# Performance work log

Hardware: AMD Instinct MI355X
Metric: run time of the kernel (lower is better)

## Reference

```python
import jax, jax.numpy as jnp
import numpy as np

K = 7        # kernel_dim
P = 3        # padding
G = 1        # groups
EPS = 1e-5   # BatchNorm eps


def _unfold(X):
    # X: (B, C, H, W) -> patches (B, C, K*K, H, W), torch.nn.Unfold ordering (C major, then kh, kw)
    B, C, H, W = X.shape
    Xp = jnp.pad(X, ((0, 0), (0, 0), (P, P), (P, P)))
    pats = [Xp[:, :, i:i + H, j:j + W] for i in range(K) for j in range(K)]
    return jnp.stack(pats, axis=2)


def setup_inputs() -> dict:
    key = jax.random.key(0)
    ks = jax.random.split(key, 4)
    B, C, H, W = 2, 64, 128, 128
    Cr = 16  # out_dim // reduction
    return {
        "X": jax.random.normal(ks[0], (B, C, H, W), dtype=jnp.float32),
        "w_reduce": jax.random.normal(ks[1], (Cr, C), dtype=jnp.float32) * 0.05,
        "b_reduce": jnp.zeros((Cr,), dtype=jnp.float32),
        "gamma": jnp.ones((Cr,), dtype=jnp.float32),
        "beta": jnp.zeros((Cr,), dtype=jnp.float32),
        "w_span": jax.random.normal(ks[2], (K * K * G, Cr), dtype=jnp.float32) * 0.05,
        "b_span": jnp.zeros((K * K * G,), dtype=jnp.float32),
    }


def reference(X, w_reduce, b_reduce, gamma, beta, w_span, b_span):
    B, C, H, W = X.shape
    out_dim = C  # in_dim == out_dim -> initial_mapping is Identity

    # unfold (im2col): (B, G, out_dim//G, K*K, H, W)
    unfolded = _unfold(X).reshape(B, G, out_dim // G, K * K, H, W)

    # kernel generation: stride==1 -> pool is Identity
    reduced = jnp.einsum('bchw,oc->bohw', X, w_reduce) + b_reduce[None, :, None, None]
    # BatchNorm2d (training mode: batch statistics) + ReLU
    mean = reduced.mean(axis=(0, 2, 3))
    var = reduced.var(axis=(0, 2, 3))
    bn = (reduced - mean[None, :, None, None]) * jax.lax.rsqrt(var + EPS)[None, :, None, None]
    act = jax.nn.relu(bn * gamma[None, :, None, None] + beta[None, :, None, None])

    kernel = jnp.einsum('bchw,kc->bkhw', act, w_span) + b_span[None, :, None, None]
    kernel = kernel.reshape(B, G, K * K, H, W)[:, :, None]  # (B, G, 1, K*K, H, W)

    out = (kernel * unfolded).sum(axis=3)  # (B, G, out_dim//G, H, W)
    return out.reshape(B, out_dim, H, W)
```

## Files before the change

kernel.cpp:

```cpp
#include <hip/hip_runtime.h>
#include <math.h>

constexpr int B  = 2, C = 64, H = 128, W = 128;
constexpr int Cr = 16;
constexpr int K  = 7, KK = 49;
constexpr int HW  = H * W;
constexpr int CHW = C * HW;
constexpr int NPIX = B * HW;
constexpr float EPS = 1e-5f;

constexpr int R_F = NPIX * Cr;
constexpr int P_F = 512 * 32;
constexpr size_t WS_NEED = (size_t)(R_F + P_F + 64) * 4;


__global__ __launch_bounds__(256) void k_reduce_r(
    const float* __restrict__ X, const float* __restrict__ w_reduce,
    const float* __restrict__ b_reduce, float* __restrict__ r_ws,
    float* __restrict__ partial)
{
    __shared__ float wrS[Cr * C];
    __shared__ float tmpA[4][Cr][64];
    const int t = threadIdx.x;
    for (int i = t; i < Cr * C; i += 256) wrS[i] = w_reduce[i];
    __syncthreads();

    const int pixl = t & 63, cg = t >> 6;
    const int p = blockIdx.x * 64 + pixl;
    const int b = p >> 14, hw = p & (HW - 1);
    const float* xb = X + (size_t)b * CHW + hw;

    float x[16];
    #pragma unroll
    for (int i = 0; i < 16; ++i) x[i] = xb[(cg * 16 + i) * HW];

    float rp[16];
    #pragma unroll
    for (int o = 0; o < 16; ++o) rp[o] = (cg == 0) ? b_reduce[o] : 0.f;
    #pragma unroll
    for (int i = 0; i < 16; ++i) {
        const float xv = x[i];
        #pragma unroll
        for (int o = 0; o < 16; ++o)
            rp[o] = fmaf(xv, wrS[o * 64 + cg * 16 + i], rp[o]);
    }
    #pragma unroll
    for (int o = 0; o < 16; ++o) tmpA[cg][o][pixl] = rp[o];
    __syncthreads();

    float rr[4];
    #pragma unroll
    for (int j = 0; j < 4; ++j) {
        const int o = cg * 4 + j;
        rr[j] = tmpA[0][o][pixl] + tmpA[1][o][pixl] + tmpA[2][o][pixl] + tmpA[3][o][pixl];
    }
    *(float4*)&r_ws[(size_t)p * 16 + cg * 4] = make_float4(rr[0], rr[1], rr[2], rr[3]);

    float s[4], q[4];
    #pragma unroll
    for (int j = 0; j < 4; ++j) { s[j] = rr[j]; q[j] = rr[j] * rr[j]; }
    #pragma unroll
    for (int off = 32; off > 0; off >>= 1) {
        #pragma unroll
        for (int j = 0; j < 4; ++j) {
            s[j] += __shfl_down(s[j], off);
            q[j] += __shfl_down(q[j], off);
        }
    }
    if ((t & 63) == 0) {
        #pragma unroll
        for (int j = 0; j < 4; ++j) {
            partial[blockIdx.x * 32 + cg * 4 + j]      = s[j];
            partial[blockIdx.x * 32 + 16 + cg * 4 + j] = q[j];
        }
    }
}

constexpr int TLH = 8, TLW = 16;
constexpr int HR = TLH + 6, HC = TLW + 6;
constexpr int RPT = 24;
constexpr int CSP = HR * RPT + 4;
constexpr int XS3_F = 32 * CSP;
constexpr int KC3_F = KK * 128;
constexpr int SMEM3_F = XS3_F + KC3_F + 256 + 32;
constexpr int SMEM3_BYTES = SMEM3_F * 4;

__global__ __launch_bounds__(256) void k_inv3(
    const float* __restrict__ X, const float* __restrict__ r_ws,
    const float* __restrict__ partial, const float* __restrict__ gamma,
    const float* __restrict__ beta, const float* __restrict__ w_span,
    const float* __restrict__ b_span, float* __restrict__ out)
{
    extern __shared__ float smem[];
    float* Xs  = smem;
    float* kcS = Xs + XS3_F;
    float* red = kcS + KC3_F;
    float* scS = red + 256;
    float* ofS = scS + 16;

    const int t   = threadIdx.x;
    const int raw = blockIdx.x;
    const int wg  = (raw & 7) * 64 + (raw >> 3);
    const int tile = wg & 127;
    const int half = (wg >> 7) & 1;
    const int b    = wg >> 8;
    const int th0 = (tile >> 3) * TLH;
    const int tw0 = (tile & 7) * TLW;

    const int px = t & 127;
    const int h  = t >> 7;
    const int p1r = px >> 4, p1c = px & 15;
    const size_t gp = (size_t)b * HW + (size_t)(th0 + p1r) * W + (tw0 + p1c);
    const float4 r0 = *(const float4*)&r_ws[gp * 16 + 0];
    const float4 r1 = *(const float4*)&r_ws[gp * 16 + 4];
    const float4 r2 = *(const float4*)&r_ws[gp * 16 + 8];
    const float4 r3 = *(const float4*)&r_ws[gp * 16 + 12];

    {
        const int scol = t & 31;
        const int sch  = t >> 5;
        const int gw   = tw0 + scol - 3;
        const bool wok = (unsigned)gw < (unsigned)W;
        const float* xg = X + (size_t)b * CHW + (size_t)(half * 32) * HW;
        #pragma unroll
        for (int cb = 0; cb < 4; ++cb) {
            const int c = cb * 8 + sch;
            const float* xc = xg + (size_t)c * HW;
            float* xs = Xs + c * CSP + scol;
            #pragma unroll
            for (int r = 0; r < HR; ++r) {
                const int gh = th0 + r - 3;
                float v = 0.f;
                if (wok && (unsigned)gh < (unsigned)H) v = xc[gh * W + gw];
                if (scol < HC) xs[r * RPT] = v;
            }
        }
    }

    {
        const int o = t & 31, seg = t >> 5;
        float acc = 0.f;
        #pragma unroll 16
        for (int j = 0; j < 64; ++j) acc += partial[(size_t)(seg * 64 + j) * 32 + o];
        red[seg * 32 + o] = acc;
    }
    __syncthreads();
    if (t < 64) {
        const int o2 = t & 31;
        float tot = 0.f;
        #pragma unroll
        for (int g = 0; g < 8; ++g) tot += red[g * 32 + o2];
        const float sq = __shfl(tot, (t & 31) + 16);
        if (t < 16) {
            const float mean = tot / (float)NPIX;
            const float var  = sq / (float)NPIX - mean * mean;
            const float sc   = gamma[t] * rsqrtf(var + EPS);
            scS[t] = sc;
            ofS[t] = beta[t] - mean * sc;
        }
    }
    __syncthreads();

    {
        float act[16];
        const float rv[16] = {r0.x, r0.y, r0.z, r0.w, r1.x, r1.y, r1.z, r1.w,
                              r2.x, r2.y, r2.z, r2.w, r3.x, r3.y, r3.z, r3.w};
        #pragma unroll
        for (int o = 0; o < 16; ++o)
            act[o] = fmaxf(fmaf(scS[o], rv[o], ofS[o]), 0.f);
        #pragma unroll
        for (int j = 0; j < 25; ++j) {
            const int k = h * 25 + j;
            if (k < KK) {
                float v = b_span[k];
                #pragma unroll
                for (int o = 0; o < 16; ++o)
                    v = fmaf(act[o], w_span[k * 16 + o], v);
                kcS[k * 128 + px] = v;
            }
        }
    }
    __syncthreads();

    const int strip = t & 31;
    const int chg   = t >> 5;
    const int pr3 = strip >> 2, pc = (strip & 3) * 4;
    const int c0  = chg * 4;

    float acc[4][4];
    #pragma unroll
    for (int i = 0; i < 4; ++i)
        #pragma unroll
        for (int j = 0; j < 4; ++j) acc[i][j] = 0.f;

    #pragma unroll
    for (int kh = 0; kh < 7; ++kh) {
        float4 kcr[7];
        #pragma unroll
        for (int kw = 0; kw < 7; ++kw)
            kcr[kw] = *(const float4*)&kcS[(kh * 7 + kw) * 128 + pr3 * 16 + pc];
        const float* kf = (const float*)kcr;
        #pragma unroll
        for (int i = 0; i < 4; ++i) {
            const float* xr = &Xs[(c0 + i) * CSP + (pr3 + kh) * RPT + pc];
            const float4 xa = *(const float4*)&xr[0];
            const float4 xb = *(const float4*)&xr[4];
            const float4 xc = *(const float4*)&xr[8];
            const float xw[12] = {xa.x, xa.y, xa.z, xa.w,
                                  xb.x, xb.y, xb.z, xb.w,
                                  xc.x, xc.y, xc.z, xc.w};
            #pragma unroll
            for (int kw = 0; kw < 7; ++kw)
                #pragma unroll
                for (int j = 0; j < 4; ++j)
                    acc[i][j] = fmaf(kf[kw * 4 + j], xw[kw + j], acc[i][j]);
        }
    }

    float* ob = out + (size_t)b * CHW + (size_t)(half * 32 + c0) * HW
                    + (size_t)(th0 + pr3) * W + (tw0 + pc);
    #pragma unroll
    for (int i = 0; i < 4; ++i)
        *(float4*)&ob[(size_t)i * HW] = make_float4(acc[i][0], acc[i][1], acc[i][2], acc[i][3]);
}


constexpr int XS_F  = C * 196;
constexpr int KC_F  = KK * 64;
constexpr int ACT_F = Cr * 64;
constexpr int WR_F  = Cr * C;
constexpr int WSP_F = KK * Cr;
constexpr int SMEM_F = XS_F + KC_F + ACT_F + WR_F + WSP_F + KK + Cr + Cr;
constexpr int SMEM_BYTES = SMEM_F * 4;

__global__ __launch_bounds__(128) void k_reduce_stats(
    const float* __restrict__ X, const float* __restrict__ w_reduce,
    const float* __restrict__ b_reduce, float* __restrict__ partial)
{
    __shared__ float wr[WR_F];
    __shared__ float brd[Cr];
    __shared__ float tmp[2][32];
    const int t = threadIdx.x;
    for (int i = t; i < WR_F; i += 128) wr[i] = w_reduce[i];
    if (t < Cr) brd[t] = b_reduce[t];
    __syncthreads();
    const int p  = blockIdx.x * 128 + t;
    const int b  = p >> 14;
    const int hw = p & (HW - 1);
    const float* xb = X + b * CHW + hw;
    float r[Cr];
    #pragma unroll
    for (int o = 0; o < Cr; ++o) r[o] = brd[o];
    #pragma unroll 4
    for (int c = 0; c < C; ++c) {
        const float x = xb[c * HW];
        #pragma unroll
        for (int o = 0; o < Cr; ++o) r[o] = fmaf(x, wr[o * C + c], r[o]);
    }
    const int lane = t & 63, wv = t >> 6;
    #pragma unroll
    for (int o = 0; o < Cr; ++o) {
        float s = r[o], q = r[o] * r[o];
        #pragma unroll
        for (int off = 32; off > 0; off >>= 1) {
            s += __shfl_down(s, off);
            q += __shfl_down(q, off);
        }
        if (lane == 0) { tmp[wv][o] = s; tmp[wv][Cr + o] = q; }
    }
    __syncthreads();
    if (t < 32) partial[blockIdx.x * 32 + t] = tmp[0][t] + tmp[1][t];
}

__global__ __launch_bounds__(256) void k_stats_final(
    const float* __restrict__ partial, float* __restrict__ stats)
{
    __shared__ float red[256];
    __shared__ float fin[32];
    const int t = threadIdx.x;
    const int o = t & 31, g = t >> 5;
    float acc = 0.f;
    #pragma unroll 8
    for (int j = 0; j < 32; ++j) acc += partial[(g * 32 + j) * 32 + o];
    red[t] = acc;
    __syncthreads();
    if (t < 32) {
        float v = 0.f;
        #pragma unroll
        for (int g2 = 0; g2 < 8; ++g2) v += red[g2 * 32 + t];
        fin[t] = v;
    }
    __syncthreads();
    if (t < Cr) {
        const float mean = fin[t] / (float)NPIX;
        const float var  = fin[Cr + t] / (float)NPIX - mean * mean;
        stats[t]      = mean;
        stats[Cr + t] = rsqrtf(var + EPS);
    }
}

__global__ __launch_bounds__(256) void k_involution(
    const float* __restrict__ X, const float* __restrict__ w_reduce,
    const float* __restrict__ b_reduce, const float* __restrict__ gamma,
    const float* __restrict__ beta, const float* __restrict__ w_span,
    const float* __restrict__ b_span, const float* __restrict__ stats,
    float* __restrict__ out)
{
    extern __shared__ float smem[];
    float* Xs   = smem;
    float* kcS  = Xs  + XS_F;
    float* actS = kcS + KC_F;
    float* wrS  = actS + ACT_F;
    float* wspS = wrS + WR_F;
    float* bspS = wspS + WSP_F;
    float* scS  = bspS + KK;
    float* ofS  = scS + Cr;
    const int t    = threadIdx.x;
    const int bx   = blockIdx.x;
    const int b    = bx >> 8;
    const int tile = bx & 255;
    const int h0   = (tile >> 4) << 3;
    const int w0   = (tile & 15) << 3;
    const float* xbg = X + b * CHW;
    for (int idx = t; idx < XS_F; idx += 256) {
        const int c   = idx / 196;
        const int rem = idx - c * 196;
        const int r   = rem / 14;
        const int col = rem - r * 14;
        const int gh  = h0 + r - 3, gw = w0 + col - 3;
        float v = 0.f;
        if ((unsigned)gh < (unsigned)H && (unsigned)gw < (unsigned)W)
            v = xbg[c * HW + gh * W + gw];
        Xs[idx] = v;
    }
    for (int i = t; i < WR_F;  i += 256) wrS[i]  = w_reduce[i];
    for (int i = t; i < WSP_F; i += 256) wspS[i] = w_span[i];
    if (t < KK) bspS[t] = b_span[t];
    if (t < Cr) {
        const float m  = stats[t];
        const float rs = stats[Cr + t];
        const float gm = gamma[t];
        scS[t] = gm * rs;
        ofS[t] = (b_reduce[t] - m) * gm * rs + beta[t];
    }
    __syncthreads();
    const int pix = t & 63;
    const int grp = t >> 6;
    const int ph  = pix >> 3, pw = pix & 7;
    {
        const int base = (ph + 3) * 14 + (pw + 3);
        float d0 = 0.f, d1 = 0.f, d2 = 0.f, d3 = 0.f;
        #pragma unroll 8
        for (int c = 0; c < C; ++c) {
            const float x = Xs[c * 196 + base];
            d0 = fmaf(x, wrS[(grp * 4 + 0) * C + c], d0);
            d1 = fmaf(x, wrS[(grp * 4 + 1) * C + c], d1);
            d2 = fmaf(x, wrS[(grp * 4 + 2) * C + c], d2);
            d3 = fmaf(x, wrS[(grp * 4 + 3) * C + c], d3);
        }
        const float d[4] = {d0, d1, d2, d3};
        #pragma unroll
        for (int j = 0; j < 4; ++j) {
            const int o = grp * 4 + j;
            actS[o * 64 + pix] = fmaxf(fmaf(scS[o], d[j], ofS[o]), 0.f);
        }
    }
    __syncthreads();
    for (int k = grp; k < KK; k += 4) {
        float v = bspS[k];
        #pragma unroll
        for (int o = 0; o < Cr; ++o)
            v = fmaf(actS[o * 64 + pix], wspS[k * Cr + o], v);
        kcS[k * 64 + pix] = v;
    }
    __syncthreads();
    float acc[16];
    #pragma unroll
    for (int i = 0; i < 16; ++i) acc[i] = 0.f;
    const float* xsc = Xs + grp * 16 * 196;
    #pragma unroll
    for (int k = 0; k < KK; ++k) {
        const int kh = k / 7, kw = k - (k / 7) * 7;
        const float kcv = kcS[k * 64 + pix];
        const int xoff = (ph + kh) * 14 + (pw + kw);
        #pragma unroll
        for (int i = 0; i < 16; ++i)
            acc[i] = fmaf(kcv, xsc[i * 196 + xoff], acc[i]);
    }
    float* ob = out + b * CHW + (grp * 16) * HW + (h0 + ph) * W + (w0 + pw);
    #pragma unroll
    for (int i = 0; i < 16; ++i) ob[i * HW] = acc[i];
}


extern "C" void kernel_launch(void* const* d_in, const int* in_sizes, int n_in,
                              void* d_out, int out_size, void* d_ws, size_t ws_size,
                              hipStream_t stream) {
    const float* X        = (const float*)d_in[0];
    const float* w_reduce = (const float*)d_in[1];
    const float* b_reduce = (const float*)d_in[2];
    const float* gamma    = (const float*)d_in[3];
    const float* beta     = (const float*)d_in[4];
    const float* w_span   = (const float*)d_in[5];
    const float* b_span   = (const float*)d_in[6];
    float* out = (float*)d_out;
    float* ws  = (float*)d_ws;

    if (ws_size >= WS_NEED) {
        float* r_ws    = ws;
        float* partial = ws + R_F;
        hipFuncSetAttribute((const void*)k_inv3,
                            hipFuncAttributeMaxDynamicSharedMemorySize, SMEM3_BYTES);
        k_reduce_r<<<512, 256, 0, stream>>>(X, w_reduce, b_reduce, r_ws, partial);
        k_inv3<<<512, 256, SMEM3_BYTES, stream>>>(X, r_ws, partial, gamma, beta,
                                                  w_span, b_span, out);
    } else {
        float* partial = ws;
        float* stats   = ws + 8192;
        hipFuncSetAttribute((const void*)k_involution,
                            hipFuncAttributeMaxDynamicSharedMemorySize, SMEM_BYTES);
        k_reduce_stats<<<256, 128, 0, stream>>>(X, w_reduce, b_reduce, partial);
        k_stats_final<<<1, 256, 0, stream>>>(partial, stats);
        k_involution<<<512, 256, SMEM_BYTES, stream>>>(
            X, w_reduce, b_reduce, gamma, beta, w_span, b_span, stats, out);
    }
}
```

Measured before the change: 35.03 us.

## Split involution kernel into quarter-channel blocks and stage span weights in LDS

The involution kernel now handles 16 channels per block instead of 32, doubling the grid to 1024 blocks and halving the X halo tile in shared memory. Each block also copies w_span and b_span into shared memory and reads them as float4, replacing repeated global scalar loads. Dynamic shared memory and the attribute call are dropped in favour of static arrays. The trade-off is that the per-pixel kernel generation (BN stats reduction and 49x16 span matmul) is now repeated across four channel groups instead of two, adding redundant work per pixel.

```diff
diff --git a/kernel.cpp b/kernel.cpp
--- a/kernel.cpp
+++ b/kernel.cpp
@@ -80,30 +80,29 @@
 constexpr int HR = TLH + 6, HC = TLW + 6;
 constexpr int RPT = 24;
 constexpr int CSP = HR * RPT + 4;
-constexpr int XS3_F = 32 * CSP;
-constexpr int KC3_F = KK * 128;
-constexpr int SMEM3_F = XS3_F + KC3_F + 256 + 32;
-constexpr int SMEM3_BYTES = SMEM3_F * 4;
-
-__global__ __launch_bounds__(256) void k_inv3(
+constexpr int XS4_F = 16 * CSP;
+constexpr int KC4_F = KK * 128;
+constexpr int WSP_F = KK * Cr;
+
+__global__ __launch_bounds__(256) void k_inv4(
     const float* __restrict__ X, const float* __restrict__ r_ws,
     const float* __restrict__ partial, const float* __restrict__ gamma,
     const float* __restrict__ beta, const float* __restrict__ w_span,
     const float* __restrict__ b_span, float* __restrict__ out)
 {
-    extern __shared__ float smem[];
-    float* Xs  = smem;
-    float* kcS = Xs + XS3_F;
-    float* red = kcS + KC3_F;
-    float* scS = red + 256;
-    float* ofS = scS + 16;
+    __shared__ float Xs[XS4_F];
+    __shared__ float kcS[KC4_F];
+    __shared__ float wspS[WSP_F];
+    __shared__ float bspS[KK + 3];
+    __shared__ float red[256];
+    __shared__ float scS[16], ofS[16];
 
     const int t   = threadIdx.x;
     const int raw = blockIdx.x;
-    const int wg  = (raw & 7) * 64 + (raw >> 3);
+    const int wg  = (raw & 7) * 128 + (raw >> 3);
     const int tile = wg & 127;
-    const int half = (wg >> 7) & 1;
-    const int b    = wg >> 8;
+    const int q    = (wg >> 7) & 3;
+    const int b    = wg >> 9;
     const int th0 = (tile >> 3) * TLH;
     const int tw0 = (tile & 7) * TLW;
 
@@ -121,9 +120,9 @@
         const int sch  = t >> 5;
         const int gw   = tw0 + scol - 3;
         const bool wok = (unsigned)gw < (unsigned)W;
-        const float* xg = X + (size_t)b * CHW + (size_t)(half * 32) * HW;
-        #pragma unroll
-        for (int cb = 0; cb < 4; ++cb) {
+        const float* xg = X + (size_t)b * CHW + (size_t)(q * 16) * HW;
+        #pragma unroll
+        for (int cb = 0; cb < 2; ++cb) {
             const int c = cb * 8 + sch;
             const float* xc = xg + (size_t)c * HW;
             float* xs = Xs + c * CSP + scol;
@@ -137,6 +136,9 @@
         }
     }
 
+    if (t < 196) *(float4*)&wspS[t * 4] = *(const float4*)&w_span[t * 4];
+    if (t >= 196 && t < 196 + KK) bspS[t - 196] = b_span[t - 196];
+
     {
         const int o = t & 31, seg = t >> 5;
         float acc = 0.f;
@@ -172,10 +174,19 @@
         for (int j = 0; j < 25; ++j) {
             const int k = h * 25 + j;
             if (k < KK) {
-                float v = b_span[k];
-                #pragma unroll
-                for (int o = 0; o < 16; ++o)
-                    v = fmaf(act[o], w_span[k * 16 + o], v);
+                const float4 w0 = *(const float4*)&wspS[k * 16 + 0];
+                const float4 w1 = *(const float4*)&wspS[k * 16 + 4];
+                const float4 w2 = *(const float4*)&wspS[k * 16 + 8];
+                const float4 w3 = *(const float4*)&wspS[k * 16 + 12];
+                float v = bspS[k];
+                v = fmaf(act[0],  w0.x, v); v = fmaf(act[1],  w0.y, v);
+                v = fmaf(act[2],  w0.z, v); v = fmaf(act[3],  w0.w, v);
+                v = fmaf(act[4],  w1.x, v); v = fmaf(act[5],  w1.y, v);
+                v = fmaf(act[6],  w1.z, v); v = fmaf(act[7],  w1.w, v);
+                v = fmaf(act[8],  w2.x, v); v = fmaf(act[9],  w2.y, v);
+                v = fmaf(act[10], w2.z, v); v = fmaf(act[11], w2.w, v);
+                v = fmaf(act[12], w3.x, v); v = fmaf(act[13], w3.y, v);
+                v = fmaf(act[14], w3.z, v); v = fmaf(act[15], w3.w, v);
                 kcS[k * 128 + px] = v;
             }
         }
@@ -185,11 +196,11 @@
     const int strip = t & 31;
     const int chg   = t >> 5;
     const int pr3 = strip >> 2, pc = (strip & 3) * 4;
-    const int c0  = chg * 4;
-
-    float acc[4][4];
-    #pragma unroll
-    for (int i = 0; i < 4; ++i)
+    const int c0  = chg * 2;
+
+    float acc[2][4];
+    #pragma unroll
+    for (int i = 0; i < 2; ++i)
         #pragma unroll
         for (int j = 0; j < 4; ++j) acc[i][j] = 0.f;
 
@@ -201,7 +212,7 @@
             kcr[kw] = *(const float4*)&kcS[(kh * 7 + kw) * 128 + pr3 * 16 + pc];
         const float* kf = (const float*)kcr;
         #pragma unroll
-        for (int i = 0; i < 4; ++i) {
+        for (int i = 0; i < 2; ++i) {
             const float* xr = &Xs[(c0 + i) * CSP + (pr3 + kh) * RPT + pc];
             const float4 xa = *(const float4*)&xr[0];
             const float4 xb = *(const float4*)&xr[4];
@@ -217,10 +228,10 @@
         }
     }
 
-    float* ob = out + (size_t)b * CHW + (size_t)(half * 32 + c0) * HW
+    float* ob = out + (size_t)b * CHW + (size_t)(q * 16 + c0) * HW
                     + (size_t)(th0 + pr3) * W + (tw0 + pc);
     #pragma unroll
-    for (int i = 0; i < 4; ++i)
+    for (int i = 0; i < 2; ++i)
         *(float4*)&ob[(size_t)i * HW] = make_float4(acc[i][0], acc[i][1], acc[i][2], acc[i][3]);
 }
 
@@ -229,7 +240,6 @@
 constexpr int KC_F  = KK * 64;
 constexpr int ACT_F = Cr * 64;
 constexpr int WR_F  = Cr * C;
-constexpr int WSP_F = KK * Cr;
 constexpr int SMEM_F = XS_F + KC_F + ACT_F + WR_F + WSP_F + KK + Cr + Cr;
 constexpr int SMEM_BYTES = SMEM_F * 4;
 
@@ -409,11 +419,9 @@
     if (ws_size >= WS_NEED) {
         float* r_ws    = ws;
         float* partial = ws + R_F;
-        hipFuncSetAttribute((const void*)k_inv3,
-                            hipFuncAttributeMaxDynamicSharedMemorySize, SMEM3_BYTES);
         k_reduce_r<<<512, 256, 0, stream>>>(X, w_reduce, b_reduce, r_ws, partial);
-        k_inv3<<<512, 256, SMEM3_BYTES, stream>>>(X, r_ws, partial, gamma, beta,
-                                                  w_span, b_span, out);
+        k_inv4<<<1024, 256, 0, stream>>>(X, r_ws, partial, gamma, beta,
+                                         w_span, b_span, out);
     } else {
         float* partial = ws;
         float* stats   = ws + 8192;
```

Result: slower. 37.52 us (+7.1%).

## Store input halo and generated kernels in fp16 shared memory with channel-pair interleave

Applied to the files above, without the earlier changes.

The involution kernel now keeps the padded input tile and the per-pixel generated 7x7 kernels in shared memory as _Float16 instead of float, interleaving channel pairs so one 32-bit LDS word carries two channels. Inner-loop FMAs still accumulate in fp32 after converting the halves. This halves LDS footprint and LDS read traffic, which can raise occupancy and cut bank pressure. It also switches to static shared memory and a readfirstlane for the kernel-row index. The cost is reduced precision in both the input and the kernel weights, plus extra conversion instructions per FMA.

```diff
diff --git a/kernel.cpp b/kernel.cpp
--- a/kernel.cpp
+++ b/kernel.cpp
@@ -12,6 +12,16 @@
 constexpr int R_F = NPIX * Cr;
 constexpr int P_F = 512 * 32;
 constexpr size_t WS_NEED = (size_t)(R_F + P_F + 64) * 4;
+
+typedef _Float16 half4v __attribute__((ext_vector_type(4)));
+typedef _Float16 v2h    __attribute__((ext_vector_type(2)));
+
+__device__ __forceinline__ float loF(unsigned u) {
+    v2h h = __builtin_bit_cast(v2h, u); return (float)h[0];
+}
+__device__ __forceinline__ float hiF(unsigned u) {
+    v2h h = __builtin_bit_cast(v2h, u); return (float)h[1];
+}
 
 
 __global__ __launch_bounds__(256) void k_reduce_r(
@@ -78,25 +88,19 @@
 
 constexpr int TLH = 8, TLW = 16;
 constexpr int HR = TLH + 6, HC = TLW + 6;
-constexpr int RPT = 24;
-constexpr int CSP = HR * RPT + 4;
-constexpr int XS3_F = 32 * CSP;
-constexpr int KC3_F = KK * 128;
-constexpr int SMEM3_F = XS3_F + KC3_F + 256 + 32;
-constexpr int SMEM3_BYTES = SMEM3_F * 4;
-
-__global__ __launch_bounds__(256) void k_inv3(
+constexpr int RPP = 44;
+constexpr int CPP = HR * RPP;
+
+__global__ __launch_bounds__(256) void k_inv7(
     const float* __restrict__ X, const float* __restrict__ r_ws,
     const float* __restrict__ partial, const float* __restrict__ gamma,
     const float* __restrict__ beta, const float* __restrict__ w_span,
     const float* __restrict__ b_span, float* __restrict__ out)
 {
-    extern __shared__ float smem[];
-    float* Xs  = smem;
-    float* kcS = Xs + XS3_F;
-    float* red = kcS + KC3_F;
-    float* scS = red + 256;
-    float* ofS = scS + 16;
+    __shared__ __align__(16) _Float16 Xs[16 * CPP];
+    __shared__ __align__(16) _Float16 kcS[KK * 128];
+    __shared__ float scS[16], ofS[16];
+    float* red = (float*)kcS;
 
     const int t   = threadIdx.x;
     const int raw = blockIdx.x;
@@ -108,7 +112,7 @@
     const int tw0 = (tile & 7) * TLW;
 
     const int px = t & 127;
-    const int h  = t >> 7;
+    const int kh2 = t >> 7;
     const int p1r = px >> 4, p1c = px & 15;
     const size_t gp = (size_t)b * HW + (size_t)(th0 + p1r) * W + (tw0 + p1c);
     const float4 r0 = *(const float4*)&r_ws[gp * 16 + 0];
@@ -120,19 +124,20 @@
         const int scol = t & 31;
         const int sch  = t >> 5;
         const int gw   = tw0 + scol - 3;
-        const bool wok = (unsigned)gw < (unsigned)W;
+        const bool ok  = ((unsigned)gw < (unsigned)W) && (scol < HC);
         const float* xg = X + (size_t)b * CHW + (size_t)(half * 32) * HW;
         #pragma unroll
         for (int cb = 0; cb < 4; ++cb) {
-            const int c = cb * 8 + sch;
+            const int c  = cb * 8 + sch;
+            const int cp = c >> 1, cl = c & 1;
             const float* xc = xg + (size_t)c * HW;
-            float* xs = Xs + c * CSP + scol;
+            _Float16* xs = Xs + cp * CPP + scol * 2 + cl;
             #pragma unroll
             for (int r = 0; r < HR; ++r) {
                 const int gh = th0 + r - 3;
                 float v = 0.f;
-                if (wok && (unsigned)gh < (unsigned)H) v = xc[gh * W + gw];
-                if (scol < HC) xs[r * RPT] = v;
+                if (ok && (unsigned)gh < (unsigned)H) v = xc[gh * W + gw];
+                if (scol < HC) xs[r * RPP] = (_Float16)v;
             }
         }
     }
@@ -168,15 +173,16 @@
         #pragma unroll
         for (int o = 0; o < 16; ++o)
             act[o] = fmaxf(fmaf(scS[o], rv[o], ofS[o]), 0.f);
+        const int kb = __builtin_amdgcn_readfirstlane(kh2) * 25;
         #pragma unroll
         for (int j = 0; j < 25; ++j) {
-            const int k = h * 25 + j;
+            const int k = kb + j;
             if (k < KK) {
+                const float* wk = w_span + k * 16;
                 float v = b_span[k];
                 #pragma unroll
-                for (int o = 0; o < 16; ++o)
-                    v = fmaf(act[o], w_span[k * 16 + o], v);
-                kcS[k * 128 + px] = v;
+                for (int o = 0; o < 16; ++o) v = fmaf(act[o], wk[o], v);
+                kcS[k * 128 + px] = (_Float16)v;
             }
         }
     }
@@ -195,25 +201,28 @@
 
     #pragma unroll
     for (int kh = 0; kh < 7; ++kh) {
-        float4 kcr[7];
+        half4v kcr[7];
         #pragma unroll
         for (int kw = 0; kw < 7; ++kw)
-            kcr[kw] = *(const float4*)&kcS[(kh * 7 + kw) * 128 + pr3 * 16 + pc];
-        const float* kf = (const float*)kcr;
-        #pragma unroll
-        for (int i = 0; i < 4; ++i) {
-            const float* xr = &Xs[(c0 + i) * CSP + (pr3 + kh) * RPT + pc];
-            const float4 xa = *(const float4*)&xr[0];
-            const float4 xb = *(const float4*)&xr[4];
-            const float4 xc = *(const float4*)&xr[8];
-            const float xw[12] = {xa.x, xa.y, xa.z, xa.w,
-                                  xb.x, xb.y, xb.z, xb.w,
-                                  xc.x, xc.y, xc.z, xc.w};
+            kcr[kw] = *(const half4v*)&kcS[(kh * 7 + kw) * 128 + pr3 * 16 + pc];
+        #pragma unroll
+        for (int dc = 0; dc < 2; ++dc) {
+            const int cp = chg * 2 + dc;
+            const _Float16* xr = &Xs[cp * CPP + (pr3 + kh) * RPP + pc * 2];
+            const uint4 xa = *(const uint4*)&xr[0];
+            const uint4 xb = *(const uint4*)&xr[8];
+            const uint4 xc = *(const uint4*)&xr[16];
+            const unsigned xu[12] = {xa.x, xa.y, xa.z, xa.w,
+                                     xb.x, xb.y, xb.z, xb.w,
+                                     xc.x, xc.y, xc.z, xc.w};
             #pragma unroll
             for (int kw = 0; kw < 7; ++kw)
                 #pragma unroll
-                for (int j = 0; j < 4; ++j)
-                    acc[i][j] = fmaf(kf[kw * 4 + j], xw[kw + j], acc[i][j]);
+                for (int j = 0; j < 4; ++j) {
+                    const float kf = (float)kcr[kw][j];
+                    acc[dc * 2 + 0][j] = fmaf(kf, loF(xu[kw + j]), acc[dc * 2 + 0][j]);
+                    acc[dc * 2 + 1][j] = fmaf(kf, hiF(xu[kw + j]), acc[dc * 2 + 1][j]);
+                }
         }
     }
 
@@ -409,11 +418,9 @@
     if (ws_size >= WS_NEED) {
         float* r_ws    = ws;
         float* partial = ws + R_F;
-        hipFuncSetAttribute((const void*)k_inv3,
-                            hipFuncAttributeMaxDynamicSharedMemorySize, SMEM3_BYTES);
         k_reduce_r<<<512, 256, 0, stream>>>(X, w_reduce, b_reduce, r_ws, partial);
-        k_inv3<<<512, 256, SMEM3_BYTES, stream>>>(X, r_ws, partial, gamma, beta,
-                                                  w_span, b_span, out);
+        k_inv7<<<512, 256, 0, stream>>>(X, r_ws, partial, gamma, beta,
+                                        w_span, b_span, out);
     } else {
         float* partial = ws;
         float* stats   = ws + 8192;
```

Result: faster. 31.30 us (-10.6%).
